# Performance work log

Hardware: AMD Instinct MI355X
Metric: run time of the kernel (lower is better)

The kernel has to match this reference:

```python
import jax, jax.numpy as jnp
import numpy as np

D_MODEL = 1024
NUM_HEADS = 16
HEAD_DIM = D_MODEL // NUM_HEADS


def setup_inputs() -> dict:
    key = jax.random.key(0)
    ks = jax.random.split(key, 11)
    B, S = 2, 2048
    s = 1.0 / np.sqrt(D_MODEL)
    inp = {
        'q': jax.random.normal(ks[0], (B, S, D_MODEL), jnp.float32),
        'k': jax.random.normal(ks[1], (B, S, D_MODEL), jnp.float32),
        'v': jax.random.normal(ks[2], (B, S, D_MODEL), jnp.float32),
        'wq': jax.random.normal(ks[3], (D_MODEL, D_MODEL), jnp.float32) * s,
        'bq': jnp.zeros((D_MODEL,), jnp.float32),
        'wk': jax.random.normal(ks[4], (D_MODEL, D_MODEL), jnp.float32) * s,
        'bk': jnp.zeros((D_MODEL,), jnp.float32),
        'wv': jax.random.normal(ks[5], (D_MODEL, D_MODEL), jnp.float32) * s,
        'bv': jnp.zeros((D_MODEL,), jnp.float32),
        'wo': jax.random.normal(ks[6], (D_MODEL, D_MODEL), jnp.float32) * s,
        'bo': jnp.zeros((D_MODEL,), jnp.float32),
    }
    return inp


def _split_heads(x, B):
    # [B, S, D] -> [B, H, S, Hd]
    return x.reshape(B, -1, NUM_HEADS, HEAD_DIM).transpose(0, 2, 1, 3)


def reference(q, k, v, wq, bq, wk, bk, wv, bv, wo, bo):
    B = q.shape[0]
    qh = _split_heads(q @ wq + bq, B)
    kh = _split_heads(k @ wk + bk, B)
    vh = _split_heads(v @ wv + bv, B)
    scale = 1.0 / np.sqrt(HEAD_DIM).astype(np.float32)
    # [B, H, Sq, Sk]
    scores = jnp.einsum('bhqd,bhkd->bhqk', qh, kh) * scale
    probs = jax.nn.softmax(scores, axis=-1)
    out = jnp.einsum('bhqk,bhkd->bhqd', probs, vh)  # [B, H, Sq, Hd]
    out = out.transpose(0, 2, 1, 3).reshape(B, -1, D_MODEL)
    return out @ wo + bo
```

## Files before the change

### kernel.cpp

```cpp
#include <hip/hip_runtime.h>

typedef unsigned short u16;
typedef __bf16 bf16x8 __attribute__((ext_vector_type(8)));
typedef float    f32x4 __attribute__((ext_vector_type(4)));
typedef float   f32x16 __attribute__((ext_vector_type(16)));
typedef u16      u16x8 __attribute__((ext_vector_type(8)));
typedef u16      u16x4 __attribute__((ext_vector_type(4)));
typedef unsigned uint4v __attribute__((ext_vector_type(4)));

#define DM 1024
#define SQ 2048
#define HD 64

__device__ __forceinline__ u16 f2bf(float f) {
    unsigned u = __builtin_bit_cast(unsigned, f);
    u += 0x7FFFu + ((u >> 16) & 1u);
    return (u16)(u >> 16);
}

__device__ __forceinline__ bf16x8 ldsbf(const u16* p) {
    return __builtin_bit_cast(bf16x8, *(const u16x8*)p);
}

__device__ __forceinline__ unsigned cvtpk(float a, float b) {
    unsigned r;
    asm("v_cvt_pk_bf16_f32 %0, %1, %2" : "=v"(r) : "v"(a), "v"(b));
    return r;
}

__device__ __forceinline__ void swap32(unsigned &a, unsigned &b) {
    asm volatile("v_permlane32_swap_b32 %0, %1" : "+v"(a), "+v"(b));
}

typedef __attribute__((address_space(3))) unsigned lds_u32_t;
typedef __attribute__((address_space(1))) const unsigned glob_u32_t;
__device__ __forceinline__ void gl_lds16(const u16* g, u16* l) {
    __builtin_amdgcn_global_load_lds((glob_u32_t*)g, (lds_u32_t*)l, 16, 0, 0);
}

__global__ __launch_bounds__(256) void convert_kernel(
    const float* __restrict__ q, const float* __restrict__ k,
    const float* __restrict__ v,
    u16* __restrict__ Qc, u16* __restrict__ Kc, u16* __restrict__ Vc)
{
    const int which = blockIdx.x >> 11;
    const float* src = (which==0) ? q : (which==1) ? k : v;
    u16* dst         = (which==0) ? Qc : (which==1) ? Kc : Vc;
    const int off = ((blockIdx.x & 2047) << 11) + threadIdx.x * 8;
    f32x4 x0 = *(const f32x4*)&src[off];
    f32x4 x1 = *(const f32x4*)&src[off + 4];
    u16x8 u;
#pragma unroll
    for (int e = 0; e < 4; ++e) { u[e] = f2bf(x0[e]); u[e+4] = f2bf(x1[e]); }
    *(u16x8*)&dst[off] = u;
}

__global__ __launch_bounds__(256) void wtrans_kernel(
    const float* __restrict__ w0, const float* __restrict__ w1,
    const float* __restrict__ w2, const float* __restrict__ w3,
    u16* __restrict__ t0, u16* __restrict__ t1,
    u16* __restrict__ t2, u16* __restrict__ t3)
{
    __shared__ float tile[32][33];
    const int z = blockIdx.z;
    const float* W = (z==0) ? w0 : (z==1) ? w1 : (z==2) ? w2 : w3;
    u16* T        = (z==0) ? t0 : (z==1) ? t1 : (z==2) ? t2 : t3;
    const int tx = threadIdx.x & 31, ty = threadIdx.x >> 5;
    const int n0 = blockIdx.x * 32, k0 = blockIdx.y * 32;
#pragma unroll
    for (int i = 0; i < 4; ++i)
        tile[ty + 8*i][tx] = W[(size_t)(k0 + ty + 8*i)*DM + n0 + tx];
    __syncthreads();
#pragma unroll
    for (int i = 0; i < 4; ++i)
        T[(size_t)(n0 + ty + 8*i)*DM + k0 + tx] = f2bf(tile[tx][ty + 8*i]);
}

template<bool OF32, bool VTLAST>
__global__ __launch_bounds__(256) void gemm_kernel(
    const u16* __restrict__ a0, const u16* __restrict__ a1, const u16* __restrict__ a2,
    const u16* __restrict__ w0, const u16* __restrict__ w1, const u16* __restrict__ w2,
    const float* __restrict__ bi0, const float* __restrict__ bi1, const float* __restrict__ bi2,
    void* __restrict__ o0, void* __restrict__ o1, void* __restrict__ o2)
{
    __shared__ __align__(16) u16 As[128*64];
    __shared__ __align__(16) u16 Bs[128*64];

    const int cpx  = gridDim.x >> 3;
    const int wgid = (blockIdx.x & 7) * cpx + (blockIdx.x >> 3);
    const int z   = wgid >> 8;
    const int rem = wgid & 255;
    const int by  = rem >> 3, bx = rem & 7;

    const u16*  Ap  = (z==0) ? a0 : (z==1) ? a1 : a2;
    const u16*  Wp  = (z==0) ? w0 : (z==1) ? w1 : w2;
    const float* Bp = (z==0) ? bi0 : (z==1) ? bi1 : bi2;
    void* Op        = (z==0) ? o0 : (z==1) ? o1 : o2;

    const int tid  = threadIdx.x;
    const int lane = tid & 63;
    const int wv   = tid >> 6;
    const int m0 = by * 128;
    const int n0 = bx * 128;
    const int wr = (wv >> 1) * 64;
    const int wc = (wv & 1) * 64;
    const int g  = lane >> 4;
    const int mm = lane & 15;

    const int l8  = lane >> 3;
    const int chs = (lane & 7) ^ l8;
    const int lrow = wv*8 + l8;

    const f32x4 zero4 = {0.f, 0.f, 0.f, 0.f};
    f32x4 acc[4][4];
#pragma unroll
    for (int i = 0; i < 4; ++i)
#pragma unroll
        for (int j = 0; j < 4; ++j) acc[i][j] = zero4;

    for (int kt = 0; kt < 16; ++kt) {
        const int k0 = kt * 64;
#pragma unroll
        for (int i = 0; i < 4; ++i) {
            const int row = i*32 + lrow;
            gl_lds16(&Ap[(size_t)(m0+row)*DM + k0 + chs*8], &As[(i*32 + wv*8)*64]);
            gl_lds16(&Wp[(size_t)(n0+row)*DM + k0 + chs*8], &Bs[(i*32 + wv*8)*64]);
        }
        __syncthreads();
#pragma unroll
        for (int ks = 0; ks < 2; ++ks) {
            bf16x8 af[4], bfr[4];
#pragma unroll
            for (int rt = 0; rt < 4; ++rt) {
                const int row = wr + rt*16 + mm;
                const int ch  = ks*4 + g;
                af[rt] = ldsbf(&As[row*64 + ((ch ^ (row & 7)) << 3)]);
            }
#pragma unroll
            for (int ct = 0; ct < 4; ++ct) {
                const int row = wc + ct*16 + mm;
                const int ch  = ks*4 + g;
                bfr[ct] = ldsbf(&Bs[row*64 + ((ch ^ (row & 7)) << 3)]);
            }
            __builtin_amdgcn_s_setprio(1);
#pragma unroll
            for (int rt = 0; rt < 4; ++rt)
#pragma unroll
                for (int ct = 0; ct < 4; ++ct)
                    acc[rt][ct] = __builtin_amdgcn_mfma_f32_16x16x32_bf16(
                        af[rt], bfr[ct], acc[rt][ct], 0, 0, 0);
            __builtin_amdgcn_s_setprio(0);
        }
        __syncthreads();
    }
    if (VTLAST && z == 2) {
#pragma unroll
        for (int ct = 0; ct < 4; ++ct) {
            const int col = n0 + wc + ct*16 + mm;
            const float bv = Bp[col];
#pragma unroll
            for (int rt = 0; rt < 4; ++rt) {
                const int row0 = m0 + wr + rt*16 + g*4;
                const int bb = row0 >> 11, s = row0 & (SQ-1);
                u16x4 pk;
#pragma unroll
                for (int r = 0; r < 4; ++r) pk[r] = f2bf(acc[rt][ct][r] + bv);
                *(u16x4*)&((u16*)Op)[(size_t)(bb*DM + col)*SQ + s] = pk;
            }
        }
    } else {
#pragma unroll
        for (int ct = 0; ct < 4; ++ct) {
            const int col = n0 + wc + ct*16 + mm;
            const float bv = Bp[col];
#pragma unroll
            for (int rt = 0; rt < 4; ++rt) {
#pragma unroll
                for (int r = 0; r < 4; ++r) {
                    const int row = m0 + wr + rt*16 + g*4 + r;
                    const float vv = acc[rt][ct][r] + bv;
                    if (OF32) ((float*)Op)[(size_t)row*DM + col] = vv;
                    else      ((u16*) Op)[(size_t)row*DM + col] = f2bf(vv);
                }
            }
        }
    }
}

__global__ __launch_bounds__(512) void attn_kernel(
    const u16* __restrict__ Q, const u16* __restrict__ K,
    const u16* __restrict__ Vt, u16* __restrict__ Z)
{
    __shared__ __align__(16) u16 Kl[2][64*64];
    __shared__ __align__(16) u16 Vl[2][64*64];

    const int tid  = threadIdx.x;
    const int lane = tid & 63;
    const int wid  = tid >> 6;
    const int c    = lane & 31;
    const int hi   = lane >> 5;
    const int q0   = blockIdx.x * 256;
    const int h    = blockIdx.y;
    const int b    = blockIdx.z;
    const int srow = tid >> 3;
    const int c8   = tid & 7;

    const size_t kbase = (size_t)(b*SQ)*DM + h*HD;
    const size_t vbase = (size_t)((b*16 + h)*HD)*SQ;

    bf16x8 qf[4];
    {
        const size_t qoff = (size_t)(b*SQ + q0 + wid*32 + c)*DM + h*HD + hi*8;
#pragma unroll
        for (int ks = 0; ks < 4; ++ks)
            qf[ks] = ldsbf(&Q[qoff + ks*16]);
    }

    f32x16 oacc[2];
#pragma unroll
    for (int dt = 0; dt < 2; ++dt)
#pragma unroll
        for (int r = 0; r < 16; ++r) oacc[dt][r] = 0.f;
    float lsum = 0.f;

    const int stw = srow*64 + ((c8 ^ (srow & 7)) << 3);
    u16x8 kreg = *(const u16x8*)&K [kbase + (size_t)srow*DM + c8*8];
    u16x8 vreg = *(const u16x8*)&Vt[vbase + (size_t)srow*SQ + c8*8];
    *(u16x8*)&Kl[0][stw] = kreg;
    *(u16x8*)&Vl[0][stw] = vreg;

    const float SC = 0.18033688f;

    for (int t = 0; t < SQ/64; ++t) {
        const int cur = t & 1;
        if (t + 1 < SQ/64) {
            kreg = *(const u16x8*)&K [kbase + (size_t)((t+1)*64 + srow)*DM + c8*8];
            vreg = *(const u16x8*)&Vt[vbase + (size_t)srow*SQ + (t+1)*64 + c8*8];
        }
        __syncthreads();

        f32x16 pacc[2];
#pragma unroll
        for (int kt = 0; kt < 2; ++kt)
#pragma unroll
            for (int r = 0; r < 16; ++r) pacc[kt][r] = 0.f;
        __builtin_amdgcn_s_setprio(1);
#pragma unroll
        for (int ks = 0; ks < 4; ++ks) {
#pragma unroll
            for (int kt = 0; kt < 2; ++kt) {
                const int row = kt*32 + c;
                const int ch  = ks*2 + hi;
                bf16x8 kf = ldsbf(&Kl[cur][row*64 + ((ch ^ (row & 7)) << 3)]);
                pacc[kt] = __builtin_amdgcn_mfma_f32_32x32x16_bf16(kf, qf[ks], pacc[kt], 0, 0, 0);
            }
        }
        __builtin_amdgcn_s_setprio(0);

        float ls = 0.f;
#pragma unroll
        for (int kt = 0; kt < 2; ++kt)
#pragma unroll
            for (int r = 0; r < 16; ++r) {
                const float e = __builtin_amdgcn_exp2f(pacc[kt][r] * SC);
                pacc[kt][r] = e;
                ls += e;
            }
        lsum += ls;

        bf16x8 pa[4];
#pragma unroll
        for (int kt = 0; kt < 2; ++kt)
#pragma unroll
            for (int k2 = 0; k2 < 2; ++k2) {
                const int bs = k2*8;
                unsigned u = cvtpk(pacc[kt][bs+0], pacc[kt][bs+1]);
                unsigned v = cvtpk(pacc[kt][bs+2], pacc[kt][bs+3]);
                unsigned w = cvtpk(pacc[kt][bs+4], pacc[kt][bs+5]);
                unsigned x = cvtpk(pacc[kt][bs+6], pacc[kt][bs+7]);
                swap32(u, w);
                swap32(v, x);
                uint4v fr = {u, v, w, x};
                pa[kt*2 + k2] = __builtin_bit_cast(bf16x8, fr);
            }

        __builtin_amdgcn_s_setprio(1);
#pragma unroll
        for (int kp = 0; kp < 4; ++kp) {
#pragma unroll
            for (int dt = 0; dt < 2; ++dt) {
                const int d  = dt*32 + c;
                const int ch = kp*2 + hi;
                bf16x8 vf = ldsbf(&Vl[cur][d*64 + ((ch ^ (d & 7)) << 3)]);
                oacc[dt] = __builtin_amdgcn_mfma_f32_32x32x16_bf16(pa[kp], vf, oacc[dt], 0, 0, 0);
            }
        }
        __builtin_amdgcn_s_setprio(0);

        if (t + 1 < SQ/64) {
            *(u16x8*)&Kl[cur^1][stw] = kreg;
            *(u16x8*)&Vl[cur^1][stw] = vreg;
        }
    }

    lsum += __shfl_xor(lsum, 32, 64);
    const float linv = 1.f / lsum;
    float linvr[16];
#pragma unroll
    for (int r = 0; r < 16; ++r)
        linvr[r] = __shfl(linv, (r & 3) + 8*(r >> 2) + 4*hi, 64);

#pragma unroll
    for (int dt = 0; dt < 2; ++dt)
#pragma unroll
        for (int r = 0; r < 16; ++r) {
            const int qrl = (r & 3) + 8*(r >> 2) + 4*hi;
            const size_t row = (size_t)(b*SQ + q0 + wid*32 + qrl);
            Z[row*DM + h*HD + dt*32 + c] = f2bf(oacc[dt][r] * linvr[r]);
        }
}

extern "C" void kernel_launch(void* const* d_in, const int* in_sizes, int n_in,
                              void* d_out, int out_size, void* d_ws, size_t ws_size,
                              hipStream_t stream)
{
    const float* q  = (const float*)d_in[0];
    const float* k  = (const float*)d_in[1];
    const float* v  = (const float*)d_in[2];
    const float* wq = (const float*)d_in[3];
    const float* bq = (const float*)d_in[4];
    const float* wk = (const float*)d_in[5];
    const float* bk = (const float*)d_in[6];
    const float* wv = (const float*)d_in[7];
    const float* bv = (const float*)d_in[8];
    const float* wo = (const float*)d_in[9];
    const float* bo = (const float*)d_in[10];
    float* out = (float*)d_out;

    char* ws = (char*)d_ws;
    u16* Qc  = (u16*)(ws);
    u16* Kc  = (u16*)(ws + 8388608);
    u16* Vc  = (u16*)(ws + 16777216);
    u16* Qb  = (u16*)(ws + 25165824);
    u16* Kb  = (u16*)(ws + 33554432);
    u16* VtB = (u16*)(ws + 41943040);
    u16* WtQ = (u16*)(ws + 50331648);
    u16* WtK = (u16*)(ws + 52428800);
    u16* WtV = (u16*)(ws + 54525952);
    u16* WtO = (u16*)(ws + 56623104);
    u16* Zb  = Qc;

    wtrans_kernel<<<dim3(32, 32, 4), 256, 0, stream>>>(
        wq, wk, wv, wo, WtQ, WtK, WtV, WtO);

    convert_kernel<<<dim3(3*2048), 256, 0, stream>>>(q, k, v, Qc, Kc, Vc);

    gemm_kernel<false, true><<<dim3(768), 256, 0, stream>>>(
        Qc, Kc, Vc, WtQ, WtK, WtV, bq, bk, bv,
        (void*)Qb, (void*)Kb, (void*)VtB);

    attn_kernel<<<dim3(SQ/256, 16, 2), 512, 0, stream>>>(Qb, Kb, VtB, Zb);

    gemm_kernel<true, false><<<dim3(256), 256, 0, stream>>>(
        Zb, Zb, Zb, WtO, WtO, WtO, bo, bo, bo,
        (void*)out, (void*)out, (void*)out);
}
```

Before: 128.4 us.

## Fold softmax scale into Wq, shrink attention blocks, remap grid and reswizzle LDS

Pre-multiplies the Q projection weights and bias by the softmax scale (log2e/sqrt(d)), removing the per-score multiply in the attention loop. The attention kernel now runs 256 threads per block over 128 query rows, launched as a 1D grid of 512 blocks remapped so related heads share an XCD. Each thread stages two K/V rows per tile, and the LDS swizzle also XORs in row>>3. The first QK MFMA starts from a zero vector instead of explicitly zeroed accumulators. Scaling Wq before the bf16 rounding changes numerics slightly, and smaller blocks double how often each K/V tile is reloaded per query.

Measured after the change: 131.3 us. 1.02x slower.

```diff
diff --git a/kernel.cpp b/kernel.cpp
--- a/kernel.cpp
+++ b/kernel.cpp
@@ -11,6 +11,9 @@
 #define DM 1024
 #define SQ 2048
 #define HD 64
+#define QSCALE 0.18033688f
+
+#define SWZ8(row, ch) ((((ch) ^ ((row) & 7) ^ ((row) >> 3)) & 7))
 
 __device__ __forceinline__ u16 f2bf(float f) {
     unsigned u = __builtin_bit_cast(unsigned, f);
@@ -65,6 +68,7 @@
     const int z = blockIdx.z;
     const float* W = (z==0) ? w0 : (z==1) ? w1 : (z==2) ? w2 : w3;
     u16* T        = (z==0) ? t0 : (z==1) ? t1 : (z==2) ? t2 : t3;
+    const float sc = (z==0) ? QSCALE : 1.0f;
     const int tx = threadIdx.x & 31, ty = threadIdx.x >> 5;
     const int n0 = blockIdx.x * 32, k0 = blockIdx.y * 32;
 #pragma unroll
@@ -73,7 +77,7 @@
     __syncthreads();
 #pragma unroll
     for (int i = 0; i < 4; ++i)
-        T[(size_t)(n0 + ty + 8*i)*DM + k0 + tx] = f2bf(tile[tx][ty + 8*i]);
+        T[(size_t)(n0 + ty + 8*i)*DM + k0 + tx] = f2bf(tile[tx][ty + 8*i] * sc);
 }
 
 template<bool OF32, bool VTLAST>
@@ -81,7 +85,8 @@
     const u16* __restrict__ a0, const u16* __restrict__ a1, const u16* __restrict__ a2,
     const u16* __restrict__ w0, const u16* __restrict__ w1, const u16* __restrict__ w2,
     const float* __restrict__ bi0, const float* __restrict__ bi1, const float* __restrict__ bi2,
-    void* __restrict__ o0, void* __restrict__ o1, void* __restrict__ o2)
+    void* __restrict__ o0, void* __restrict__ o1, void* __restrict__ o2,
+    float bscale0)
 {
     __shared__ __align__(16) u16 As[128*64];
     __shared__ __align__(16) u16 Bs[128*64];
@@ -96,6 +101,7 @@
     const u16*  Wp  = (z==0) ? w0 : (z==1) ? w1 : w2;
     const float* Bp = (z==0) ? bi0 : (z==1) ? bi1 : bi2;
     void* Op        = (z==0) ? o0 : (z==1) ? o1 : o2;
+    const float bsc = (z==0) ? bscale0 : 1.0f;
 
     const int tid  = threadIdx.x;
     const int lane = tid & 63;
@@ -157,7 +163,7 @@
 #pragma unroll
         for (int ct = 0; ct < 4; ++ct) {
             const int col = n0 + wc + ct*16 + mm;
-            const float bv = Bp[col];
+            const float bv = Bp[col] * bsc;
 #pragma unroll
             for (int rt = 0; rt < 4; ++rt) {
                 const int row0 = m0 + wr + rt*16 + g*4;
@@ -172,7 +178,7 @@
 #pragma unroll
         for (int ct = 0; ct < 4; ++ct) {
             const int col = n0 + wc + ct*16 + mm;
-            const float bv = Bp[col];
+            const float bv = Bp[col] * bsc;
 #pragma unroll
             for (int rt = 0; rt < 4; ++rt) {
 #pragma unroll
@@ -187,7 +193,7 @@
     }
 }
 
-__global__ __launch_bounds__(512) void attn_kernel(
+__global__ __launch_bounds__(256) void attn_kernel(
     const u16* __restrict__ Q, const u16* __restrict__ K,
     const u16* __restrict__ Vt, u16* __restrict__ Z)
 {
@@ -199,11 +205,15 @@
     const int wid  = tid >> 6;
     const int c    = lane & 31;
     const int hi   = lane >> 5;
-    const int q0   = blockIdx.x * 256;
-    const int h    = blockIdx.y;
-    const int b    = blockIdx.z;
     const int srow = tid >> 3;
     const int c8   = tid & 7;
+
+    const int wg = (blockIdx.x & 7) * 64 + (blockIdx.x >> 3);
+    const int qt = wg & 15;
+    const int hb = wg >> 4;
+    const int h  = hb & 15;
+    const int b  = hb >> 4;
+    const int q0 = qt * 128;
 
     const size_t kbase = (size_t)(b*SQ)*DM + h*HD;
     const size_t vbase = (size_t)((b*16 + h)*HD)*SQ;
@@ -221,37 +231,50 @@
     for (int dt = 0; dt < 2; ++dt)
 #pragma unroll
         for (int r = 0; r < 16; ++r) oacc[dt][r] = 0.f;
+    f32x16 z16;
+#pragma unroll
+    for (int r = 0; r < 16; ++r) z16[r] = 0.f;
     float lsum = 0.f;
 
-    const int stw = srow*64 + ((c8 ^ (srow & 7)) << 3);
-    u16x8 kreg = *(const u16x8*)&K [kbase + (size_t)srow*DM + c8*8];
-    u16x8 vreg = *(const u16x8*)&Vt[vbase + (size_t)srow*SQ + c8*8];
-    *(u16x8*)&Kl[0][stw] = kreg;
-    *(u16x8*)&Vl[0][stw] = vreg;
-
-    const float SC = 0.18033688f;
+    int stw[2];
+    u16x8 kreg[2], vreg[2];
+#pragma unroll
+    for (int p = 0; p < 2; ++p) {
+        const int row = p*32 + srow;
+        stw[p] = row*64 + (SWZ8(row, c8) << 3);
+        kreg[p] = *(const u16x8*)&K [kbase + (size_t)row*DM + c8*8];
+        vreg[p] = *(const u16x8*)&Vt[vbase + (size_t)row*SQ + c8*8];
+        *(u16x8*)&Kl[0][stw[p]] = kreg[p];
+        *(u16x8*)&Vl[0][stw[p]] = vreg[p];
+    }
 
     for (int t = 0; t < SQ/64; ++t) {
         const int cur = t & 1;
         if (t + 1 < SQ/64) {
-            kreg = *(const u16x8*)&K [kbase + (size_t)((t+1)*64 + srow)*DM + c8*8];
-            vreg = *(const u16x8*)&Vt[vbase + (size_t)srow*SQ + (t+1)*64 + c8*8];
+#pragma unroll
+            for (int p = 0; p < 2; ++p) {
+                const int row = p*32 + srow;
+                kreg[p] = *(const u16x8*)&K [kbase + (size_t)((t+1)*64 + row)*DM + c8*8];
+                vreg[p] = *(const u16x8*)&Vt[vbase + (size_t)row*SQ + (t+1)*64 + c8*8];
+            }
         }
         __syncthreads();
 
         f32x16 pacc[2];
-#pragma unroll
-        for (int kt = 0; kt < 2; ++kt)
-#pragma unroll
-            for (int r = 0; r < 16; ++r) pacc[kt][r] = 0.f;
         __builtin_amdgcn_s_setprio(1);
 #pragma unroll
-        for (int ks = 0; ks < 4; ++ks) {
+        for (int kt = 0; kt < 2; ++kt) {
+            const int row = kt*32 + c;
+            bf16x8 kf = ldsbf(&Kl[cur][row*64 + (SWZ8(row, hi) << 3)]);
+            pacc[kt] = __builtin_amdgcn_mfma_f32_32x32x16_bf16(kf, qf[0], z16, 0, 0, 0);
+        }
+#pragma unroll
+        for (int ks = 1; ks < 4; ++ks) {
 #pragma unroll
             for (int kt = 0; kt < 2; ++kt) {
                 const int row = kt*32 + c;
                 const int ch  = ks*2 + hi;
-                bf16x8 kf = ldsbf(&Kl[cur][row*64 + ((ch ^ (row & 7)) << 3)]);
+                bf16x8 kf = ldsbf(&Kl[cur][row*64 + (SWZ8(row, ch) << 3)]);
                 pacc[kt] = __builtin_amdgcn_mfma_f32_32x32x16_bf16(kf, qf[ks], pacc[kt], 0, 0, 0);
             }
         }
@@ -262,7 +285,7 @@
         for (int kt = 0; kt < 2; ++kt)
 #pragma unroll
             for (int r = 0; r < 16; ++r) {
-                const float e = __builtin_amdgcn_exp2f(pacc[kt][r] * SC);
+                const float e = __builtin_amdgcn_exp2f(pacc[kt][r]);
                 pacc[kt][r] = e;
                 ls += e;
             }
@@ -291,15 +314,18 @@
             for (int dt = 0; dt < 2; ++dt) {
                 const int d  = dt*32 + c;
                 const int ch = kp*2 + hi;
-                bf16x8 vf = ldsbf(&Vl[cur][d*64 + ((ch ^ (d & 7)) << 3)]);
+                bf16x8 vf = ldsbf(&Vl[cur][d*64 + (SWZ8(d, ch) << 3)]);
                 oacc[dt] = __builtin_amdgcn_mfma_f32_32x32x16_bf16(pa[kp], vf, oacc[dt], 0, 0, 0);
             }
         }
         __builtin_amdgcn_s_setprio(0);
 
         if (t + 1 < SQ/64) {
-            *(u16x8*)&Kl[cur^1][stw] = kreg;
-            *(u16x8*)&Vl[cur^1][stw] = vreg;
+#pragma unroll
+            for (int p = 0; p < 2; ++p) {
+                *(u16x8*)&Kl[cur^1][stw[p]] = kreg[p];
+                *(u16x8*)&Vl[cur^1][stw[p]] = vreg[p];
+            }
         }
     }
 
@@ -357,11 +383,11 @@
 
     gemm_kernel<false, true><<<dim3(768), 256, 0, stream>>>(
         Qc, Kc, Vc, WtQ, WtK, WtV, bq, bk, bv,
-        (void*)Qb, (void*)Kb, (void*)VtB);
-
-    attn_kernel<<<dim3(SQ/256, 16, 2), 512, 0, stream>>>(Qb, Kb, VtB, Zb);
+        (void*)Qb, (void*)Kb, (void*)VtB, QSCALE);
+
+    attn_kernel<<<dim3(512), 256, 0, stream>>>(Qb, Kb, VtB, Zb);
 
     gemm_kernel<true, false><<<dim3(256), 256, 0, stream>>>(
         Zb, Zb, Zb, WtO, WtO, WtO, bo, bo, bo,
-        (void*)out, (void*)out, (void*)out);
-}
+        (void*)out, (void*)out, (void*)out, 1.0f);
+}
```
